# Optimization experiments

Hardware: AMD Instinct MI355X
Metric: run time of the kernel (lower is better)

The kernel has to match this reference:

```python
import jax, jax.numpy as jnp
import numpy as np

FLTRSTDEV = 2.0
EXTGRADFAC = 10.0
DMAX = 15.0
ENHANCEMENT = 2.0   # enhancement_factor in the module
NEG_WEIGHT = 1.5    # negative_weight in the module


def make_gauss_edge_fltr(stdev: float) -> np.ndarray:
    """Gaussian-derivative edge filter, shape [2, 1, k, k] (OIHW), k = 2*ceil(2*stdev)+1."""
    r = int(np.ceil(2.0 * stdev))
    x = np.arange(-r, r + 1, dtype=np.float32)
    g = np.exp(-x ** 2 / (2.0 * stdev ** 2)).astype(np.float32)
    g /= g.sum()
    dg = (-x / (stdev ** 2)) * np.exp(-x ** 2 / (2.0 * stdev ** 2))
    dg = (dg / np.abs(dg).sum()).astype(np.float32)
    f_dy = np.outer(dg, g)   # gradient along axis 0
    f_dx = np.outer(g, dg)   # gradient along axis 1
    return np.stack([f_dy, f_dx])[:, None]  # [2,1,k,k]


def cmpt_grad_im(img, fltr):
    """img: [B,1,H,W], fltr: [2,1,k,k] -> [B,2,H,W] gradient image (SAME conv)."""
    return jax.lax.conv_general_dilated(
        img, fltr, window_strides=(1, 1), padding='SAME',
        dimension_numbers=('NCHW', 'OIHW', 'NCHW'))


def setup_inputs() -> dict:
    key = jax.random.key(0)
    k1, k2 = jax.random.split(key)
    B, H, W = 16, 1024, 1024
    # predicted signed distance map, roughly in [-DMAX, DMAX]
    pred_dmap = jax.random.normal(k1, (B, 1, H, W), dtype=jnp.float32) * 5.0
    # stand-in for the snake-rendered signed distance map (detached target)
    snake_dm = jax.random.normal(k2, (B, 1, H, W), dtype=jnp.float32) * 5.0
    fltr = jnp.asarray(make_gauss_edge_fltr(FLTRSTDEV))
    return {"pred_dmap": pred_dmap, "snake_dm": snake_dm, "fltr": fltr}


def reference(pred_dmap, snake_dm, fltr):
    # external-energy gradient images driving the snakes
    gimg = cmpt_grad_im(pred_dmap, fltr) * EXTGRADFAC           # [B,2,H,W]
    gimgW = cmpt_grad_im(jnp.abs(pred_dmap), fltr) * EXTGRADFAC  # [B,2,H,W]
    # dmap[dmap > 0] = dmax  (background set to +dmax)
    sd = jnp.where(snake_dm > 0, DMAX, snake_dm)
    # snake_dm[snake_dm < 0] *= enhancement_factor
    sd = jnp.where(sd < 0, sd * ENHANCEMENT, sd)
    neg_mask = (sd < 0).astype(pred_dmap.dtype)
    squared_diff = (pred_dmap - jax.lax.stop_gradient(sd)) ** 2
    loss = jnp.mean(squared_diff * (1.0 + neg_mask * NEG_WEIGHT))
    return loss, gimg, gimgW
```

## Files before the change

kernel.cpp:

```cpp
#include <hip/hip_runtime.h>

#define HH 1024
#define WW 1024
#define BB 16
#define RR 4
#define TY 32
#define TX 64
#define LW (TX + 8)
#define DMAXC 15.0f
#define ENHC 2.0f
#define NEGWC 1.5f
#define EGFC 10.0f

__device__ __forceinline__ void fma4(float4& a, float c, const float4& v) {
    a.x += c * v.x; a.y += c * v.y; a.z += c * v.z; a.w += c * v.w;
}

__device__ __forceinline__ float4 hconv(const float* __restrict__ row, int xg,
                                        const float (&cf)[9]) {
    float w[12];
    *(float4*)&w[0] = *(const float4*)&row[xg];
    *(float4*)&w[4] = *(const float4*)&row[xg + 4];
    *(float4*)&w[8] = *(const float4*)&row[xg + 8];
    float4 acc = make_float4(0.f, 0.f, 0.f, 0.f);
#pragma unroll
    for (int j = 0; j < 9; ++j) {
        float c = cf[j];
        acc.x += c * w[j];
        acc.y += c * w[j + 1];
        acc.z += c * w[j + 2];
        acc.w += c * w[j + 3];
    }
    return acc;
}

__device__ __forceinline__ float lossterm(float p, float s) {
    float sd = (s > 0.f) ? DMAXC : s;
    sd = (sd < 0.f) ? sd * ENHC : sd;
    float w = (sd < 0.f) ? (1.f + NEGWC) : 1.f;
    float d = p - sd;
    return d * d * w;
}

__global__ __launch_bounds__(256) void snake_fused(
    const float* __restrict__ pred, const float* __restrict__ snake,
    const float* __restrict__ fltr, float* __restrict__ out) {
    __shared__ float s_in[(TY + 8) * LW];
    __shared__ float s_vA[TY * LW];
    __shared__ float s_vB[TY * LW];
    __shared__ float s_wA[TY * LW];
    __shared__ float s_wB[TY * LW];
    __shared__ float s_dg[9];
    __shared__ float s_g[9];
    __shared__ float s_red[4];

    const int t = threadIdx.x;
    const int gx0 = blockIdx.x * TX;
    const int gy0 = blockIdx.y * TY;
    const int b = blockIdx.z;
    const float* img = pred + (size_t)b * (HH * WW);

    if (t < 9) {
        float s = 0.f;
#pragma unroll
        for (int j = 0; j < 9; ++j) s += fltr[t * 9 + j];
        s_dg[t] = s;
    }
    __syncthreads();
    if (t < 9) s_g[t] = fltr[t] / s_dg[0];

    for (int idx = t; idx < (TY + 8) * LW; idx += 256) {
        int yy = idx / LW;
        int xx = idx - yy * LW;
        int gy = gy0 + yy - RR;
        int gx = gx0 + xx - RR;
        float v = 0.f;
        if ((unsigned)gy < HH && (unsigned)gx < WW) v = img[(size_t)gy * WW + gx];
        s_in[idx] = v;
    }
    __syncthreads();

    float dgr[9], gr[9];
#pragma unroll
    for (int i = 0; i < 9; ++i) { dgr[i] = s_dg[i]; gr[i] = s_g[i]; }

    for (int gidx = t; gidx < TY * (LW / 4); gidx += 256) {
        int y = gidx / (LW / 4);
        int xg = (gidx - y * (LW / 4)) * 4;
        float4 a = make_float4(0.f, 0.f, 0.f, 0.f);
        float4 bb = a, wa = a, wb = a;
#pragma unroll
        for (int i = 0; i < 9; ++i) {
            float4 v = *(const float4*)&s_in[(y + i) * LW + xg];
            float4 av = make_float4(fabsf(v.x), fabsf(v.y), fabsf(v.z), fabsf(v.w));
            fma4(a, dgr[i], v);
            fma4(bb, gr[i], v);
            fma4(wa, dgr[i], av);
            fma4(wb, gr[i], av);
        }
        *(float4*)&s_vA[y * LW + xg] = a;
        *(float4*)&s_vB[y * LW + xg] = bb;
        *(float4*)&s_wA[y * LW + xg] = wa;
        *(float4*)&s_wB[y * LW + xg] = wb;
    }
    __syncthreads();

    float lsum = 0.f;
    float* gimg = out + 1;
    float* gimgW = out + 1 + (size_t)BB * 2 * HH * WW;
    const float* snk = snake + (size_t)b * (HH * WW);

    for (int gidx = t; gidx < TY * (TX / 4); gidx += 256) {
        int y = gidx >> 4;
        int xg = (gidx & 15) * 4;
        const int ro = y * LW;
        float4 dy = hconv(&s_vA[ro], xg, gr);
        float4 dx = hconv(&s_vB[ro], xg, dgr);
        float4 dyW = hconv(&s_wA[ro], xg, gr);
        float4 dxW = hconv(&s_wB[ro], xg, dgr);

        int gy = gy0 + y, gx = gx0 + xg;
        size_t p0 = ((size_t)(b * 2 + 0)) * (HH * WW) + (size_t)gy * WW + gx;
        size_t p1 = ((size_t)(b * 2 + 1)) * (HH * WW) + (size_t)gy * WW + gx;
        gimg[p0 + 0] = EGFC * dy.x;  gimg[p0 + 1] = EGFC * dy.y;
        gimg[p0 + 2] = EGFC * dy.z;  gimg[p0 + 3] = EGFC * dy.w;
        gimg[p1 + 0] = EGFC * dx.x;  gimg[p1 + 1] = EGFC * dx.y;
        gimg[p1 + 2] = EGFC * dx.z;  gimg[p1 + 3] = EGFC * dx.w;
        gimgW[p0 + 0] = EGFC * dyW.x; gimgW[p0 + 1] = EGFC * dyW.y;
        gimgW[p0 + 2] = EGFC * dyW.z; gimgW[p0 + 3] = EGFC * dyW.w;
        gimgW[p1 + 0] = EGFC * dxW.x; gimgW[p1 + 1] = EGFC * dxW.y;
        gimgW[p1 + 2] = EGFC * dxW.z; gimgW[p1 + 3] = EGFC * dxW.w;

        float4 pv = *(const float4*)&s_in[(y + RR) * LW + xg + RR];
        float4 sv = *(const float4*)&snk[(size_t)gy * WW + gx];
        lsum += lossterm(pv.x, sv.x) + lossterm(pv.y, sv.y) +
                lossterm(pv.z, sv.z) + lossterm(pv.w, sv.w);
    }

#pragma unroll
    for (int off = 32; off > 0; off >>= 1) lsum += __shfl_down(lsum, off);
    if ((t & 63) == 0) s_red[t >> 6] = lsum;
    __syncthreads();
    if (t == 0) {
        float tot = s_red[0] + s_red[1] + s_red[2] + s_red[3];
        atomicAdd(out, tot * (1.0f / 16777216.0f));
    }
}

extern "C" void kernel_launch(void* const* d_in, const int* in_sizes, int n_in,
                              void* d_out, int out_size, void* d_ws, size_t ws_size,
                              hipStream_t stream) {
    const float* pred = (const float*)d_in[0];
    const float* snake = (const float*)d_in[1];
    const float* fltr = (const float*)d_in[2];
    float* out = (float*)d_out;

    hipMemsetAsync(out, 0, sizeof(float), stream);

    dim3 grid(WW / TX, HH / TY, BB);
    snake_fused<<<grid, 256, 0, stream>>>(pred, snake, fltr, out);
}
```

Measured before the change: 474.1 us.

## Halve tile height, vectorize halo loads, fold gradient scale into filters

Reduces the tile height from 32 to 16 rows so each 256-thread block computes exactly one output float4 per thread, and sets a launch-bounds occupancy hint of 6 blocks. The halo load into shared memory now uses float4 global loads instead of scalar loads. The EXTGRADFAC multiply is folded into the filter coefficients, removing 16 multiplies per thread. The smaller tile raises the halo overhead (24 of 40 rows instead of 40 of 72) and adds more blocks, in exchange for smaller shared-memory use and higher occupancy.

```diff
diff --git a/kernel.cpp b/kernel.cpp
--- a/kernel.cpp
+++ b/kernel.cpp
@@ -4,13 +4,12 @@
 #define WW 1024
 #define BB 16
 #define RR 4
-#define TY 32
+#define TY 16
 #define TX 64
 #define LW (TX + 8)
 #define DMAXC 15.0f
 #define ENHC 2.0f
 #define NEGWC 1.5f
-#define EGFC 10.0f
 
 __device__ __forceinline__ void fma4(float4& a, float c, const float4& v) {
     a.x += c * v.x; a.y += c * v.y; a.z += c * v.z; a.w += c * v.w;
@@ -42,7 +41,7 @@
     return d * d * w;
 }
 
-__global__ __launch_bounds__(256) void snake_fused(
+__global__ __launch_bounds__(256, 6) void snake_fused(
     const float* __restrict__ pred, const float* __restrict__ snake,
     const float* __restrict__ fltr, float* __restrict__ out) {
     __shared__ float s_in[(TY + 8) * LW];
@@ -64,19 +63,20 @@
         float s = 0.f;
 #pragma unroll
         for (int j = 0; j < 9; ++j) s += fltr[t * 9 + j];
-        s_dg[t] = s;
+        s_dg[t] = 10.0f * s;
     }
     __syncthreads();
-    if (t < 9) s_g[t] = fltr[t] / s_dg[0];
+    if (t < 9) s_g[t] = 10.0f * fltr[t] / s_dg[0];
 
-    for (int idx = t; idx < (TY + 8) * LW; idx += 256) {
-        int yy = idx / LW;
-        int xx = idx - yy * LW;
+    for (int g = t; g < (TY + 8) * (LW / 4); g += 256) {
+        int yy = g / (LW / 4);
+        int xg = (g - yy * (LW / 4)) * 4;
         int gy = gy0 + yy - RR;
-        int gx = gx0 + xx - RR;
-        float v = 0.f;
-        if ((unsigned)gy < HH && (unsigned)gx < WW) v = img[(size_t)gy * WW + gx];
-        s_in[idx] = v;
+        int gx = gx0 + xg - RR;
+        float4 v = make_float4(0.f, 0.f, 0.f, 0.f);
+        if ((unsigned)gy < HH && (unsigned)gx < WW)
+            v = *(const float4*)&img[(size_t)gy * WW + gx];
+        *(float4*)&s_in[yy * LW + xg] = v;
     }
     __syncthreads();
 
@@ -84,9 +84,9 @@
 #pragma unroll
     for (int i = 0; i < 9; ++i) { dgr[i] = s_dg[i]; gr[i] = s_g[i]; }
 
-    for (int gidx = t; gidx < TY * (LW / 4); gidx += 256) {
-        int y = gidx / (LW / 4);
-        int xg = (gidx - y * (LW / 4)) * 4;
+    for (int g = t; g < TY * (LW / 4); g += 256) {
+        int y = g / (LW / 4);
+        int xg = (g - y * (LW / 4)) * 4;
         float4 a = make_float4(0.f, 0.f, 0.f, 0.f);
         float4 bb = a, wa = a, wb = a;
 #pragma unroll
@@ -110,9 +110,9 @@
     float* gimgW = out + 1 + (size_t)BB * 2 * HH * WW;
     const float* snk = snake + (size_t)b * (HH * WW);
 
-    for (int gidx = t; gidx < TY * (TX / 4); gidx += 256) {
-        int y = gidx >> 4;
-        int xg = (gidx & 15) * 4;
+    {
+        int y = t >> 4;
+        int xg = (t & 15) * 4;
         const int ro = y * LW;
         float4 dy = hconv(&s_vA[ro], xg, gr);
         float4 dx = hconv(&s_vB[ro], xg, dgr);
@@ -122,14 +122,14 @@
         int gy = gy0 + y, gx = gx0 + xg;
         size_t p0 = ((size_t)(b * 2 + 0)) * (HH * WW) + (size_t)gy * WW + gx;
         size_t p1 = ((size_t)(b * 2 + 1)) * (HH * WW) + (size_t)gy * WW + gx;
-        gimg[p0 + 0] = EGFC * dy.x;  gimg[p0 + 1] = EGFC * dy.y;
-        gimg[p0 + 2] = EGFC * dy.z;  gimg[p0 + 3] = EGFC * dy.w;
-        gimg[p1 + 0] = EGFC * dx.x;  gimg[p1 + 1] = EGFC * dx.y;
-        gimg[p1 + 2] = EGFC * dx.z;  gimg[p1 + 3] = EGFC * dx.w;
-        gimgW[p0 + 0] = EGFC * dyW.x; gimgW[p0 + 1] = EGFC * dyW.y;
-        gimgW[p0 + 2] = EGFC * dyW.z; gimgW[p0 + 3] = EGFC * dyW.w;
-        gimgW[p1 + 0] = EGFC * dxW.x; gimgW[p1 + 1] = EGFC * dxW.y;
-        gimgW[p1 + 2] = EGFC * dxW.z; gimgW[p1 + 3] = EGFC * dxW.w;
+        gimg[p0 + 0] = dy.x;  gimg[p0 + 1] = dy.y;
+        gimg[p0 + 2] = dy.z;  gimg[p0 + 3] = dy.w;
+        gimg[p1 + 0] = dx.x;  gimg[p1 + 1] = dx.y;
+        gimg[p1 + 2] = dx.z;  gimg[p1 + 3] = dx.w;
+        gimgW[p0 + 0] = dyW.x; gimgW[p0 + 1] = dyW.y;
+        gimgW[p0 + 2] = dyW.z; gimgW[p0 + 3] = dyW.w;
+        gimgW[p1 + 0] = dxW.x; gimgW[p1 + 1] = dxW.y;
+        gimgW[p1 + 2] = dxW.z; gimgW[p1 + 3] = dxW.w;
 
         float4 pv = *(const float4*)&s_in[(y + RR) * LW + xg + RR];
         float4 sv = *(const float4*)&snk[(size_t)gy * WW + gx];
```

New measurement: 574.3 us. +21.1%, slower.
